# Performance work log

Measured on AMD Instinct MI355X. Metric: run time of the kernel, lower is better.

Reference implementation:

```python
import jax, jax.numpy as jnp
import numpy as np

# Module hyperparameters (match init_kwargs)
B, S, DM = 4, 2048, 512
H, DH = 8, 64          # num_heads, d_head; d_output = H*DH = 512
DOUT = H * DH
W, NS = 8, 2           # window, num_sinks


def setup_inputs() -> dict:
    key = jax.random.key(0)
    ks = jax.random.split(key, 7)
    x = jax.random.normal(ks[0], (B, S, DM), jnp.float32)
    sink = jax.random.normal(ks[1], (B, NS, DM), jnp.float32)
    # Learned params: key (with bias), query, value (no bias), relative-position bias
    Wk = jax.random.normal(ks[2], (DM, DOUT), jnp.float32) * 0.04
    bk = jax.random.normal(ks[3], (DOUT,), jnp.float32) * 0.02
    Wq = jax.random.normal(ks[4], (DM, DOUT), jnp.float32) * 0.04
    Wv = jax.random.normal(ks[5], (DM, DOUT), jnp.float32) * 0.04
    position = jax.random.normal(ks[6], (1, 1, DH, W + NS, 1), jnp.float32)
    return {"x": x, "sink": sink, "Wk": Wk, "bk": bk, "Wq": Wq, "Wv": Wv,
            "position": position}


def _skew(t):
    """Equivalent of RelativeAttention.skew_repeat, done with a gather
    instead of repeat/reshape. t: [B,H,DH,NS+S].
    Returns (skewed [B,H,DH,NS+W,S], valid [W,S] bool).
    skewed[..., NS+r, s] = t_main[..., r+s] if r+s < S else 0;
    skewed[..., p, s]    = t_sink[..., p]   for p < NS (broadcast over s).
    """
    sink_rows = jnp.broadcast_to(t[..., :NS][..., None],
                                 t.shape[:3] + (NS, S))       # [B,H,DH,NS,S]
    main = t[..., NS:]                                        # [B,H,DH,S]
    idx = jnp.arange(W)[:, None] + jnp.arange(S)[None, :]     # [W,S]
    valid = idx < S
    g = jnp.take(main, jnp.minimum(idx, S - 1), axis=-1)      # [B,H,DH,W,S]
    g = jnp.where(valid, g, jnp.zeros((), g.dtype))
    return jnp.concatenate([sink_rows, g], axis=3), valid


def reference(x, sink, Wk, bk, Wq, Wv, position):
    # prepend sink tokens
    xc = jnp.concatenate([sink, x], axis=1)                   # [B, NS+S, DM]

    def proj(Wm, b=None):
        y = xc @ Wm
        if b is not None:
            y = y + b
        # [B, NS+S, H, DH] -> [B, H, DH, NS+S]
        return y.reshape(B, NS + S, H, DH).transpose(0, 2, 3, 1)

    k = proj(Wk, bk)[..., NS:]                                # [B,H,DH,S] (sinks dropped)
    q = proj(Wq)
    v = proj(Wv)

    q_sk, valid = _skew(q)                                    # [B,H,DH,NS+W,S]
    q_sk = q_sk + position
    # per-dimension scores: qk[b,h,d,r,s] = q_sk[b,h,d,r,s] * k[b,h,d,s]
    qk = q_sk * k[:, :, :, None, :]                           # [B,H,DH,NS+W,S]
    # mask the skew-padding positions (r + s >= S) in the window rows; sink rows valid
    row_valid = jnp.concatenate([jnp.ones((NS, S), bool), valid], axis=0)  # [NS+W,S]
    qk = jnp.where(row_valid, qk, -jnp.inf)
    attn = jax.nn.softmax(qk, axis=3)                         # softmax over window+sink rows

    v_sk, _ = _skew(v)                                        # [B,H,DH,NS+W,S]
    out = jnp.einsum('bhdrs,bhdrs->bhds', attn, v_sk)         # [B,H,DH,S]
    # [B, d_output, S] -> [B, S, d_output]; dropout is identity in eval mode
    return out.reshape(B, DOUT, S).transpose(0, 2, 1)
```

## Files before the change

### kernel.cpp

```cpp
#include <hip/hip_runtime.h>
#include <hip/hip_bf16.h>
#include <math.h>
#include <stdint.h>

#define B_ 4
#define S_ 2048
#define DM_ 512
#define H_ 8
#define DH_ 64
#define DOUT_ 512
#define W_ 8
#define NS_ 2
#define T_ (NS_ + S_)
#define M_TOT (B_ * T_)
#define M_PAD 8320
#define N3 1536
#define SCHUNK 16

typedef __attribute__((ext_vector_type(8))) __bf16   bf16x8;
typedef __attribute__((ext_vector_type(4))) float    f32x4;
typedef __attribute__((ext_vector_type(8))) uint16_t u16x8;

__device__ inline uint16_t f2bf(float f) {
    uint32_t u = __builtin_bit_cast(uint32_t, f);
    u += 0x7FFF + ((u >> 16) & 1);
    return (uint16_t)(u >> 16);
}
__device__ inline float bf2f(uint16_t u) {
    return __builtin_bit_cast(float, (uint32_t)u << 16);
}

__global__ __launch_bounds__(256) void convA(
    const float* __restrict__ x, const float* __restrict__ sink,
    uint16_t* __restrict__ Abf)
{
    size_t id = (size_t)blockIdx.x * 256 + threadIdx.x;
    size_t e0 = id * 8;
    int row = (int)(e0 >> 9);
    int col = (int)(e0 & 511);
    u16x8 o;
    if (row < M_TOT) {
        int b = row / T_;
        int t = row - b * T_;
        const float* src = (t < NS_)
            ? &sink[((size_t)b * NS_ + t) * DM_ + col]
            : &x[((size_t)b * S_ + (t - NS_)) * DM_ + col];
        float4 v0 = *(const float4*)src;
        float4 v1 = *(const float4*)(src + 4);
        o[0] = f2bf(v0.x); o[1] = f2bf(v0.y); o[2] = f2bf(v0.z); o[3] = f2bf(v0.w);
        o[4] = f2bf(v1.x); o[5] = f2bf(v1.y); o[6] = f2bf(v1.z); o[7] = f2bf(v1.w);
    } else {
        o = (u16x8)0;
    }
    *(u16x8*)&Abf[e0] = o;
}

__global__ __launch_bounds__(256) void convB(
    const float* __restrict__ Wq, const float* __restrict__ Wk,
    const float* __restrict__ Wv, uint16_t* __restrict__ Bt)
{
    __shared__ float tile[32][65];
    const int n0 = blockIdx.x * 64, k0 = blockIdx.y * 32;
    const float* Wsrc = (n0 < 512) ? Wq : ((n0 < 1024) ? Wk : Wv);
    const int nb = n0 & 511;
    const int tid = threadIdx.x;
    const int nn = tid & 63, kk = tid >> 6;
    #pragma unroll
    for (int i = 0; i < 8; ++i)
        tile[kk + i * 4][nn] = Wsrc[(size_t)(k0 + kk + i * 4) * DOUT_ + nb + nn];
    __syncthreads();
    const int nn2 = tid >> 2, k8 = (tid & 3) * 8;
    u16x8 o;
    #pragma unroll
    for (int j = 0; j < 8; ++j) o[j] = f2bf(tile[k8 + j][nn2]);
    *(u16x8*)&Bt[(size_t)(n0 + nn2) * DM_ + k0 + k8] = o;
}

__global__ __launch_bounds__(256) void gemm_bf16(
    const uint16_t* __restrict__ Abf, const uint16_t* __restrict__ Bt,
    const float* __restrict__ bk, uint16_t* __restrict__ y)
{
    __shared__ __align__(16) uint16_t As[128 * 32];
    __shared__ __align__(16) uint16_t Bs[128 * 32];
    __shared__ __align__(16) uint16_t Ep[4][16 * 72];
    const int tid  = threadIdx.x;
    const int wave = tid >> 6, lane = tid & 63;
    const int row0 = blockIdx.y * 128, col0 = blockIdx.x * 128;
    const int wm = wave >> 1, wn = wave & 1;
    f32x4 acc[4][4] = {};

    const int srow  = tid >> 2;
    const int sslot = tid & 3;

    for (int k0 = 0; k0 < DM_; k0 += 32) {
        #pragma unroll
        for (int i = 0; i < 2; ++i) {
            const int r  = i * 64 + srow;
            const int ls = sslot ^ ((r >> 1) & 3);
            const uint16_t* ga = Abf + (size_t)(row0 + r) * DM_ + k0 + ls * 8;
            const uint16_t* gb = Bt  + (size_t)(col0 + r) * DM_ + k0 + ls * 8;
            __builtin_amdgcn_global_load_lds(
                (const __attribute__((address_space(1))) void*)ga,
                (__attribute__((address_space(3))) void*)(As + i * 2048 + wave * 512),
                16, 0, 0);
            __builtin_amdgcn_global_load_lds(
                (const __attribute__((address_space(1))) void*)gb,
                (__attribute__((address_space(3))) void*)(Bs + i * 2048 + wave * 512),
                16, 0, 0);
        }
        __syncthreads();

        const int kslot = lane >> 4;
        const int fr    = lane & 15;
        bf16x8 af[4], bfr[4];
        #pragma unroll
        for (int mi = 0; mi < 4; ++mi) {
            const int r  = wm * 64 + mi * 16 + fr;
            const int ss = kslot ^ ((r >> 1) & 3);
            af[mi] = *(const bf16x8*)&As[r * 32 + ss * 8];
        }
        #pragma unroll
        for (int ni = 0; ni < 4; ++ni) {
            const int r  = wn * 64 + ni * 16 + fr;
            const int ss = kslot ^ ((r >> 1) & 3);
            bfr[ni] = *(const bf16x8*)&Bs[r * 32 + ss * 8];
        }
        #pragma unroll
        for (int mi = 0; mi < 4; ++mi)
            #pragma unroll
            for (int ni = 0; ni < 4; ++ni)
                acc[mi][ni] = __builtin_amdgcn_mfma_f32_16x16x32_bf16(
                    af[mi], bfr[ni], acc[mi][ni], 0, 0, 0);
        __syncthreads();
    }

    const int fr = lane & 15, fq = lane >> 4;
    float bias[4];
    #pragma unroll
    for (int ni = 0; ni < 4; ++ni) {
        const int col = col0 + wn * 64 + ni * 16 + fr;
        bias[ni] = (col >= 512 && col < 1024) ? bk[col - 512] : 0.f;
    }
    const int rrow = lane >> 3;
    const int rcol = (lane & 7) * 8;
    uint16_t* ep = Ep[wave];
    #pragma unroll
    for (int mi = 0; mi < 4; ++mi) {
        #pragma unroll
        for (int ni = 0; ni < 4; ++ni)
            #pragma unroll
            for (int r4 = 0; r4 < 4; ++r4)
                ep[(fq * 4 + r4) * 72 + ni * 16 + fr] =
                    f2bf(acc[mi][ni][r4] + bias[ni]);
        __builtin_amdgcn_s_waitcnt(0);
        #pragma unroll
        for (int it = 0; it < 2; ++it) {
            const int rl  = it * 8 + rrow;
            const int row = row0 + wm * 64 + mi * 16 + rl;
            u16x8 v = *(const u16x8*)&ep[rl * 72 + rcol];
            if (row < M_TOT)
                *(u16x8*)&y[(size_t)row * N3 + col0 + wn * 64 + rcol] = v;
        }
        __builtin_amdgcn_s_waitcnt(0);
    }
}

__global__ __launch_bounds__(512) void attn_kernel(
    const uint16_t* __restrict__ y, const float* __restrict__ pos,
    float* __restrict__ out)
{
    __shared__ float spos[DH_ * (NS_ + W_)];
    for (int i = threadIdx.x; i < DH_ * (NS_ + W_); i += 512) spos[i] = pos[i];
    __syncthreads();

    const int c  = threadIdx.x;
    const int b  = blockIdx.y;
    const int s0 = blockIdx.x * SCHUNK;
    const uint16_t* yb = y + (size_t)b * T_ * N3;
    const int dh = c & (DH_ - 1);

    float pp[NS_ + W_];
    #pragma unroll
    for (int p = 0; p < NS_ + W_; ++p) pp[p] = spos[dh * (NS_ + W_) + p];

    const float sq0 = bf2f(yb[0 * N3 + c]),        sq1 = bf2f(yb[1 * N3 + c]);
    const float sv0 = bf2f(yb[0 * N3 + 1024 + c]), sv1 = bf2f(yb[1 * N3 + 1024 + c]);

    float qr[W_], vr[W_];
    #pragma unroll
    for (int j = 0; j < W_ - 1; ++j) {
        const uint16_t* rq = yb + (size_t)(NS_ + s0 + j) * N3 + c;
        qr[j] = bf2f(rq[0]);
        vr[j] = bf2f(rq[1024]);
    }

    for (int i = 0; i < SCHUNK; ++i) {
        const int s = s0 + i;
        int tq = NS_ + s + (W_ - 1);
        if (tq > T_ - 1) tq = T_ - 1;
        const uint16_t* rq = yb + (size_t)tq * N3 + c;
        qr[W_ - 1] = bf2f(rq[0]);
        vr[W_ - 1] = bf2f(rq[1024]);
        const float kv = bf2f(yb[(size_t)(NS_ + s) * N3 + 512 + c]);

        float sc[NS_ + W_];
        sc[0] = (sq0 + pp[0]) * kv;
        sc[1] = (sq1 + pp[1]) * kv;
        #pragma unroll
        for (int r = 0; r < W_; ++r) sc[NS_ + r] = (qr[r] + pp[NS_ + r]) * kv;
        if (s > S_ - W_) {
            const int nv = S_ - s;
            #pragma unroll
            for (int r = 0; r < W_; ++r)
                if (r >= nv) sc[NS_ + r] = -INFINITY;
        }

        float m = sc[0];
        #pragma unroll
        for (int p = 1; p < NS_ + W_; ++p) m = fmaxf(m, sc[p]);
        float e[NS_ + W_], sum = 0.f;
        #pragma unroll
        for (int p = 0; p < NS_ + W_; ++p) { e[p] = __expf(sc[p] - m); sum += e[p]; }
        float accv = e[0] * sv0 + e[1] * sv1;
        #pragma unroll
        for (int r = 0; r < W_; ++r) accv = fmaf(e[NS_ + r], vr[r], accv);

        out[((size_t)b * S_ + s) * DOUT_ + c] = accv / sum;

        #pragma unroll
        for (int j = 0; j < W_ - 1; ++j) { qr[j] = qr[j + 1]; vr[j] = vr[j + 1]; }
    }
}

extern "C" void kernel_launch(void* const* d_in, const int* in_sizes, int n_in,
                              void* d_out, int out_size, void* d_ws, size_t ws_size,
                              hipStream_t stream) {
    const float* x    = (const float*)d_in[0];
    const float* sink = (const float*)d_in[1];
    const float* Wk   = (const float*)d_in[2];
    const float* bk   = (const float*)d_in[3];
    const float* Wq   = (const float*)d_in[4];
    const float* Wv   = (const float*)d_in[5];
    const float* pos  = (const float*)d_in[6];

    char* ws = (char*)d_ws;
    uint16_t* y   = (uint16_t*)ws;
    uint16_t* Abf = (uint16_t*)(ws + (size_t)M_TOT * N3 * 2);
    uint16_t* Bt  = (uint16_t*)(ws + (size_t)M_TOT * N3 * 2
                                   + (size_t)M_PAD * DM_ * 2);

    convA<<<dim3(M_PAD * DM_ / 8 / 256), 256, 0, stream>>>(x, sink, Abf);
    convB<<<dim3(N3 / 64, DM_ / 32), 256, 0, stream>>>(Wq, Wk, Wv, Bt);
    gemm_bf16<<<dim3(N3 / 128, M_PAD / 128), 256, 0, stream>>>(Abf, Bt, bk, y);
    attn_kernel<<<dim3(S_ / SCHUNK, B_), 512, 0, stream>>>(y, pos, (float*)d_out);
}
```

Measured before the change: 60.58 us.

## Double-buffer GEMM LDS staging and merge input conversion kernels

The bf16 GEMM now keeps two LDS buffers, issuing the global-to-LDS loads for the next K slice before computing the current one. A partial vmcnt wait plus barriers replaces the old load/sync/compute/sync sequence. Separately, the activation and weight conversion kernels are merged into one launch, selected by block index, to save a kernel launch. LDS use doubles, which may lower occupancy, and the hand-written vmcnt count has to match the number of outstanding loads.

```diff
diff --git a/kernel.cpp b/kernel.cpp
--- a/kernel.cpp
+++ b/kernel.cpp
@@ -16,6 +16,7 @@
 #define M_PAD 8320
 #define N3 1536
 #define SCHUNK 16
+#define NBLK_A 2080
 
 typedef __attribute__((ext_vector_type(8))) __bf16   bf16x8;
 typedef __attribute__((ext_vector_type(4))) float    f32x4;
@@ -30,58 +31,58 @@
     return __builtin_bit_cast(float, (uint32_t)u << 16);
 }
 
-__global__ __launch_bounds__(256) void convA(
+__global__ __launch_bounds__(256) void conv_fused(
     const float* __restrict__ x, const float* __restrict__ sink,
-    uint16_t* __restrict__ Abf)
-{
-    size_t id = (size_t)blockIdx.x * 256 + threadIdx.x;
-    size_t e0 = id * 8;
-    int row = (int)(e0 >> 9);
-    int col = (int)(e0 & 511);
-    u16x8 o;
-    if (row < M_TOT) {
-        int b = row / T_;
-        int t = row - b * T_;
-        const float* src = (t < NS_)
-            ? &sink[((size_t)b * NS_ + t) * DM_ + col]
-            : &x[((size_t)b * S_ + (t - NS_)) * DM_ + col];
-        float4 v0 = *(const float4*)src;
-        float4 v1 = *(const float4*)(src + 4);
-        o[0] = f2bf(v0.x); o[1] = f2bf(v0.y); o[2] = f2bf(v0.z); o[3] = f2bf(v0.w);
-        o[4] = f2bf(v1.x); o[5] = f2bf(v1.y); o[6] = f2bf(v1.z); o[7] = f2bf(v1.w);
-    } else {
-        o = (u16x8)0;
-    }
-    *(u16x8*)&Abf[e0] = o;
-}
-
-__global__ __launch_bounds__(256) void convB(
     const float* __restrict__ Wq, const float* __restrict__ Wk,
-    const float* __restrict__ Wv, uint16_t* __restrict__ Bt)
+    const float* __restrict__ Wv,
+    uint16_t* __restrict__ Abf, uint16_t* __restrict__ Bt)
 {
     __shared__ float tile[32][65];
-    const int n0 = blockIdx.x * 64, k0 = blockIdx.y * 32;
-    const float* Wsrc = (n0 < 512) ? Wq : ((n0 < 1024) ? Wk : Wv);
-    const int nb = n0 & 511;
-    const int tid = threadIdx.x;
-    const int nn = tid & 63, kk = tid >> 6;
-    #pragma unroll
-    for (int i = 0; i < 8; ++i)
-        tile[kk + i * 4][nn] = Wsrc[(size_t)(k0 + kk + i * 4) * DOUT_ + nb + nn];
-    __syncthreads();
-    const int nn2 = tid >> 2, k8 = (tid & 3) * 8;
-    u16x8 o;
-    #pragma unroll
-    for (int j = 0; j < 8; ++j) o[j] = f2bf(tile[k8 + j][nn2]);
-    *(u16x8*)&Bt[(size_t)(n0 + nn2) * DM_ + k0 + k8] = o;
+    if (blockIdx.x < NBLK_A) {
+        size_t id = (size_t)blockIdx.x * 256 + threadIdx.x;
+        size_t e0 = id * 8;
+        int row = (int)(e0 >> 9);
+        int col = (int)(e0 & 511);
+        u16x8 o;
+        if (row < M_TOT) {
+            int b = row / T_;
+            int t = row - b * T_;
+            const float* src = (t < NS_)
+                ? &sink[((size_t)b * NS_ + t) * DM_ + col]
+                : &x[((size_t)b * S_ + (t - NS_)) * DM_ + col];
+            float4 v0 = *(const float4*)src;
+            float4 v1 = *(const float4*)(src + 4);
+            o[0] = f2bf(v0.x); o[1] = f2bf(v0.y); o[2] = f2bf(v0.z); o[3] = f2bf(v0.w);
+            o[4] = f2bf(v1.x); o[5] = f2bf(v1.y); o[6] = f2bf(v1.z); o[7] = f2bf(v1.w);
+        } else {
+            o = (u16x8)0;
+        }
+        *(u16x8*)&Abf[e0] = o;
+    } else {
+        const int bx = blockIdx.x - NBLK_A;
+        const int n0 = (bx % 24) * 64, k0 = (bx / 24) * 32;
+        const float* Wsrc = (n0 < 512) ? Wq : ((n0 < 1024) ? Wk : Wv);
+        const int nb = n0 & 511;
+        const int tid = threadIdx.x;
+        const int nn = tid & 63, kk = tid >> 6;
+        #pragma unroll
+        for (int i = 0; i < 8; ++i)
+            tile[kk + i * 4][nn] = Wsrc[(size_t)(k0 + kk + i * 4) * DOUT_ + nb + nn];
+        __syncthreads();
+        const int nn2 = tid >> 2, k8 = (tid & 3) * 8;
+        u16x8 o;
+        #pragma unroll
+        for (int j = 0; j < 8; ++j) o[j] = f2bf(tile[k8 + j][nn2]);
+        *(u16x8*)&Bt[(size_t)(n0 + nn2) * DM_ + k0 + k8] = o;
+    }
 }
 
 __global__ __launch_bounds__(256) void gemm_bf16(
     const uint16_t* __restrict__ Abf, const uint16_t* __restrict__ Bt,
     const float* __restrict__ bk, uint16_t* __restrict__ y)
 {
-    __shared__ __align__(16) uint16_t As[128 * 32];
-    __shared__ __align__(16) uint16_t Bs[128 * 32];
+    __shared__ __align__(16) uint16_t As[2][128 * 32];
+    __shared__ __align__(16) uint16_t Bs[2][128 * 32];
     __shared__ __align__(16) uint16_t Ep[4][16 * 72];
     const int tid  = threadIdx.x;
     const int wave = tid >> 6, lane = tid & 63;
@@ -92,7 +93,8 @@
     const int srow  = tid >> 2;
     const int sslot = tid & 3;
 
-    for (int k0 = 0; k0 < DM_; k0 += 32) {
+    auto STAGE = [&](int ks, int d) {
+        const int k0 = ks * 32;
         #pragma unroll
         for (int i = 0; i < 2; ++i) {
             const int r  = i * 64 + srow;
@@ -101,29 +103,31 @@
             const uint16_t* gb = Bt  + (size_t)(col0 + r) * DM_ + k0 + ls * 8;
             __builtin_amdgcn_global_load_lds(
                 (const __attribute__((address_space(1))) void*)ga,
-                (__attribute__((address_space(3))) void*)(As + i * 2048 + wave * 512),
+                (__attribute__((address_space(3))) void*)(&As[d][0] + i * 2048 + wave * 512),
                 16, 0, 0);
             __builtin_amdgcn_global_load_lds(
                 (const __attribute__((address_space(1))) void*)gb,
-                (__attribute__((address_space(3))) void*)(Bs + i * 2048 + wave * 512),
+                (__attribute__((address_space(3))) void*)(&Bs[d][0] + i * 2048 + wave * 512),
                 16, 0, 0);
         }
-        __syncthreads();
-
-        const int kslot = lane >> 4;
-        const int fr    = lane & 15;
+    };
+
+    const int kslot = lane >> 4;
+    const int fr    = lane & 15;
+
+    auto COMPUTE = [&](int cur) {
         bf16x8 af[4], bfr[4];
         #pragma unroll
         for (int mi = 0; mi < 4; ++mi) {
             const int r  = wm * 64 + mi * 16 + fr;
             const int ss = kslot ^ ((r >> 1) & 3);
-            af[mi] = *(const bf16x8*)&As[r * 32 + ss * 8];
+            af[mi] = *(const bf16x8*)&As[cur][r * 32 + ss * 8];
         }
         #pragma unroll
         for (int ni = 0; ni < 4; ++ni) {
             const int r  = wn * 64 + ni * 16 + fr;
             const int ss = kslot ^ ((r >> 1) & 3);
-            bfr[ni] = *(const bf16x8*)&Bs[r * 32 + ss * 8];
+            bfr[ni] = *(const bf16x8*)&Bs[cur][r * 32 + ss * 8];
         }
         #pragma unroll
         for (int mi = 0; mi < 4; ++mi)
@@ -131,10 +135,29 @@
             for (int ni = 0; ni < 4; ++ni)
                 acc[mi][ni] = __builtin_amdgcn_mfma_f32_16x16x32_bf16(
                     af[mi], bfr[ni], acc[mi][ni], 0, 0, 0);
-        __syncthreads();
-    }
-
-    const int fr = lane & 15, fq = lane >> 4;
+    };
+
+    STAGE(0, 0);
+    for (int ks = 0; ks < 15; ++ks) {
+        const int cur = ks & 1;
+        STAGE(ks + 1, cur ^ 1);
+        asm volatile("s_waitcnt vmcnt(4)" ::: "memory");
+        __builtin_amdgcn_s_barrier();
+        __builtin_amdgcn_sched_barrier(0);
+        COMPUTE(cur);
+        __builtin_amdgcn_sched_barrier(0);
+        __builtin_amdgcn_s_barrier();
+    }
+    {
+        asm volatile("s_waitcnt vmcnt(0)" ::: "memory");
+        __builtin_amdgcn_s_barrier();
+        __builtin_amdgcn_sched_barrier(0);
+        COMPUTE(1);
+        __builtin_amdgcn_sched_barrier(0);
+        __builtin_amdgcn_s_barrier();
+    }
+
+    const int fq = lane >> 4;
     float bias[4];
     #pragma unroll
     for (int ni = 0; ni < 4; ++ni) {
@@ -249,8 +272,7 @@
     uint16_t* Bt  = (uint16_t*)(ws + (size_t)M_TOT * N3 * 2
                                    + (size_t)M_PAD * DM_ * 2);
 
-    convA<<<dim3(M_PAD * DM_ / 8 / 256), 256, 0, stream>>>(x, sink, Abf);
-    convB<<<dim3(N3 / 64, DM_ / 32), 256, 0, stream>>>(Wq, Wk, Wv, Bt);
+    conv_fused<<<dim3(NBLK_A + 384), 256, 0, stream>>>(x, sink, Wq, Wk, Wv, Abf, Bt);
     gemm_bf16<<<dim3(N3 / 128, M_PAD / 128), 256, 0, stream>>>(Abf, Bt, bk, y);
     attn_kernel<<<dim3(S_ / SCHUNK, B_), 512, 0, stream>>>(y, pos, (float*)d_out);
 }
```

After: 56.96 us. 1.06x faster.
